# Kernel optimization log

Hardware: AMD Instinct MI355X
Metric: run time of the kernel (lower is better)

Reference implementation:

```python
import jax, jax.numpy as jnp
import numpy as np

B, S, D = 8, 2048, 512

def setup_inputs() -> dict:
    key = jax.random.key(0)
    k1, k2 = jax.random.split(key)
    lstm_out = jax.random.normal(k1, (B, S, D), dtype=jnp.float32)
    # xavier_uniform init for [D, D]
    limit = float(np.sqrt(6.0 / (D + D)))
    attention_weights = jax.random.uniform(k2, (D, D), dtype=jnp.float32, minval=-limit, maxval=limit)
    return {"lstm_out": lstm_out, "attention_weights": attention_weights}

def reference(lstm_out, attention_weights):
    # scores[b,i,j] = tanh( (x W) x^T )
    proj = jnp.einsum('bsd,de->bse', lstm_out, attention_weights)          # [B,S,D]
    scores = jnp.tanh(jnp.einsum('bsd,btd->bst', proj, lstm_out))          # [B,S,S]
    attn = jax.nn.softmax(scores, axis=-1)                                 # [B,S,S]
    return jnp.einsum('bst,btd->bsd', attn, lstm_out)                      # [B,S,D]
```

## Files before the change

kernel.cpp:

```cpp
#include <hip/hip_runtime.h>
#include <hip/hip_bf16.h>

typedef __bf16 bf16;
typedef __attribute__((ext_vector_type(8))) __bf16 bf16x8;
typedef __attribute__((ext_vector_type(4))) __bf16 bf16x4;
typedef __attribute__((ext_vector_type(4))) float floatx4;

__device__ __forceinline__ void gl_lds16(const bf16* g, bf16* l) {
    __builtin_amdgcn_global_load_lds(
        (const __attribute__((address_space(1))) unsigned int*)g,
        (__attribute__((address_space(3))) unsigned int*)l,
        16, 0, 0);
}

__global__ __launch_bounds__(256) void cast_f32_bf16_v4(const float* __restrict__ in,
                                                        bf16* __restrict__ out,
                                                        long long n4) {
    long long i = (long long)blockIdx.x * 256 + threadIdx.x;
    if (i < n4) {
        float4 v = ((const float4*)in)[i];
        bf16x4 o;
        o[0] = (bf16)v.x; o[1] = (bf16)v.y; o[2] = (bf16)v.z; o[3] = (bf16)v.w;
        ((bf16x4*)out)[i] = o;
    }
}

__global__ __launch_bounds__(256) void cast_transpose(const float* __restrict__ in,
                                                      bf16* __restrict__ out,
                                                      int R, int C) {
    __shared__ float tile[32][33];
    const long long bz = blockIdx.z;
    in  += bz * (long long)R * C;
    out += bz * (long long)R * C;
    const int r0 = blockIdx.x * 32, c0 = blockIdx.y * 32;
    const int tx = threadIdx.x & 31, ty = threadIdx.x >> 5;
#pragma unroll
    for (int i = 0; i < 32; i += 8)
        tile[ty + i][tx] = in[(long long)(r0 + ty + i) * C + (c0 + tx)];
    __syncthreads();
#pragma unroll
    for (int i = 0; i < 32; i += 8)
        out[(long long)(c0 + ty + i) * R + (r0 + tx)] = (bf16)tile[tx][ty + i];
}

__device__ __forceinline__ float fast_tanh(float v) {
    float e = __expf(2.0f * v);
    return 1.0f - 2.0f / (e + 1.0f);
}

template <bool TANH, bool OUTBF16>
__global__ __launch_bounds__(256) void gemm128_nt(const bf16* __restrict__ A,
                                                  const bf16* __restrict__ Bm,
                                                  void* __restrict__ Cout,
                                                  int M, int N, int K,
                                                  long long batchA, long long batchB, long long batchC) {
    const long long bz = blockIdx.z;
    A  += bz * batchA;
    Bm += bz * batchB;

    __shared__ bf16 As[128 * 32];
    __shared__ bf16 Bs[128 * 32];

    const int t    = threadIdx.x;
    const int lane = t & 63;
    const int wave = t >> 6;
    const int quad = lane >> 4;
    const int l16  = lane & 15;

    const int m0 = blockIdx.x * 128;
    const int n0 = blockIdx.y * 128;
    const int wm = (wave >> 1) * 64;
    const int wn = (wave & 1) * 64;

    floatx4 acc[4][4] = {};

    const int r0 = t >> 2;
    const int c0 = (t & 3) * 8;

    const bf16* Ag0 = A + (long long)(m0 + r0) * K + c0;
    const bf16* Ag1 = A + (long long)(m0 + 64 + r0) * K + c0;
    const bf16* Bg0 = Bm + (long long)(n0 + r0) * K + c0;
    const bf16* Bg1 = Bm + (long long)(n0 + 64 + r0) * K + c0;

    for (int k0 = 0; k0 < K; k0 += 32) {
        gl_lds16(Ag0 + k0, &As[t * 8]);
        gl_lds16(Ag1 + k0, &As[(t + 256) * 8]);
        gl_lds16(Bg0 + k0, &Bs[t * 8]);
        gl_lds16(Bg1 + k0, &Bs[(t + 256) * 8]);
        __syncthreads();

        bf16x8 af[4], bfr[4];
#pragma unroll
        for (int i = 0; i < 4; ++i)
            af[i] = *(const bf16x8*)(&As[(wm + i * 16 + l16) * 32 + quad * 8]);
#pragma unroll
        for (int j = 0; j < 4; ++j)
            bfr[j] = *(const bf16x8*)(&Bs[(wn + j * 16 + l16) * 32 + quad * 8]);

#pragma unroll
        for (int i = 0; i < 4; ++i)
#pragma unroll
            for (int j = 0; j < 4; ++j)
                acc[i][j] = __builtin_amdgcn_mfma_f32_16x16x32_bf16(af[i], bfr[j], acc[i][j], 0, 0, 0);

        __syncthreads();
    }

#pragma unroll
    for (int i = 0; i < 4; ++i) {
#pragma unroll
        for (int j = 0; j < 4; ++j) {
#pragma unroll
            for (int r = 0; r < 4; ++r) {
                long long row = m0 + wm + i * 16 + quad * 4 + r;
                long long col = n0 + wn + j * 16 + l16;
                float v = acc[i][j][r];
                if (TANH) v = fast_tanh(v);
                if (OUTBF16)
                    ((bf16*)Cout)[bz * batchC + row * (long long)N + col] = (bf16)v;
                else
                    ((float*)Cout)[bz * batchC + row * (long long)N + col] = v;
            }
        }
    }
}

__device__ __forceinline__ float waveRedMax(float v) {
#pragma unroll
    for (int o = 32; o > 0; o >>= 1) v = fmaxf(v, __shfl_xor(v, o));
    return v;
}
__device__ __forceinline__ float waveRedSum(float v) {
#pragma unroll
    for (int o = 32; o > 0; o >>= 1) v += __shfl_xor(v, o);
    return v;
}

__global__ __launch_bounds__(256) void softmax2048(bf16* __restrict__ Sb, long long batchS) {
    bf16* row = Sb + blockIdx.z * batchS + (long long)blockIdx.x * 2048;
    const int t = threadIdx.x;
    const int lane = t & 63, wave = t >> 6;

    bf16x8 pack = ((const bf16x8*)row)[t];
    float v[8];
    float mx = -1e30f;
#pragma unroll
    for (int j = 0; j < 8; ++j) { v[j] = (float)pack[j]; mx = fmaxf(mx, v[j]); }

    __shared__ float smax[4], ssum[4];
    mx = waveRedMax(mx);
    if (lane == 0) smax[wave] = mx;
    __syncthreads();
    mx = fmaxf(fmaxf(smax[0], smax[1]), fmaxf(smax[2], smax[3]));

    float s = 0.f;
#pragma unroll
    for (int j = 0; j < 8; ++j) { v[j] = __expf(v[j] - mx); s += v[j]; }
    s = waveRedSum(s);
    if (lane == 0) ssum[wave] = s;
    __syncthreads();
    s = ssum[0] + ssum[1] + ssum[2] + ssum[3];
    float inv = 1.0f / s;

    bf16x8 o;
#pragma unroll
    for (int j = 0; j < 8; ++j) o[j] = (bf16)(v[j] * inv);
    ((bf16x8*)row)[t] = o;
}

extern "C" void kernel_launch(void* const* d_in, const int* in_sizes, int n_in,
                              void* d_out, int out_size, void* d_ws, size_t ws_size,
                              hipStream_t stream) {
    const int B = 8, S = 2048, D = 512;
    const float* x = (const float*)d_in[0];
    const float* W = (const float*)d_in[1];
    float* out = (float*)d_out;

    const size_t nx = (size_t)B * S * D;
    const size_t nw = (size_t)D * D;

    char* ws = (char*)d_ws;
    auto al = [](size_t v) { return (v + 255) & ~(size_t)255; };
    size_t off = 0;
    bf16* xb = (bf16*)(ws + off); off = al(off + nx * 2);
    bf16* xt = (bf16*)(ws + off); off = al(off + nx * 2);
    bf16* pb = (bf16*)(ws + off); off = al(off + nx * 2);
    bf16* wt = (bf16*)(ws + off); off = al(off + nw * 2);
    bf16* sb = (bf16*)(ws + off);
    const size_t full_need = off + (size_t)B * S * S * 2;
    const bool batched = (ws_size >= full_need);

    cast_f32_bf16_v4<<<(int)((nx / 4 + 255) / 256), 256, 0, stream>>>(x, xb, (long long)(nx / 4));
    { dim3 g(S / 32, D / 32, B); cast_transpose<<<g, 256, 0, stream>>>(x, xt, S, D); }
    { dim3 g(D / 32, D / 32, 1); cast_transpose<<<g, 256, 0, stream>>>(W, wt, D, D); }

    {
        dim3 g(B * S / 128, D / 128, 1);
        gemm128_nt<false, true><<<g, 256, 0, stream>>>(xb, wt, (void*)pb, B * S, D, D, 0, 0, 0);
    }

    const long long sd = (long long)S * D;
    const long long ss = (long long)S * S;

    if (batched) {
        dim3 g2(S / 128, S / 128, B);
        gemm128_nt<true, true><<<g2, 256, 0, stream>>>(pb, xb, (void*)sb, S, S, D, sd, sd, ss);
        dim3 g3(S, 1, B);
        softmax2048<<<g3, 256, 0, stream>>>(sb, ss);
        dim3 g4(S / 128, D / 128, B);
        gemm128_nt<false, false><<<g4, 256, 0, stream>>>(sb, xt, (void*)out, S, D, S, ss, sd, sd);
    } else {
        for (int b = 0; b < B; ++b) {
            dim3 g2(S / 128, S / 128, 1);
            gemm128_nt<true, true><<<g2, 256, 0, stream>>>(pb + (size_t)b * sd, xb + (size_t)b * sd,
                                                          (void*)sb, S, S, D, 0, 0, 0);
            dim3 g3(S, 1, 1);
            softmax2048<<<g3, 256, 0, stream>>>(sb, 0);
            dim3 g4(S / 128, D / 128, 1);
            gemm128_nt<false, false><<<g4, 256, 0, stream>>>(sb, xt + (size_t)b * sd,
                                                             (void*)(out + (size_t)b * sd), S, D, S, 0, 0, 0);
        }
    }
}
```

Measured before the change: 248.0 us.

## Fuse softmax into score GEMM epilogue with atomic row sums and deferred normalization

Drops the separate softmax kernel. The score GEMM now writes exp(tanh(s)) and atomically accumulates per-row sums, and the output GEMM divides by the row sum in its epilogue. This is safe without max subtraction because tanh bounds the scores to [-1,1]. Both epilogues are also staged through LDS so global stores are coalesced and vectorized. The cost is extra atomics, a memset, and a larger LDS allocation that may reduce occupancy.

New measurement: 248.8 us. About the same (+0.3%).

```diff
diff --git a/kernel.cpp b/kernel.cpp
--- a/kernel.cpp
+++ b/kernel.cpp
@@ -48,18 +48,21 @@
     return 1.0f - 2.0f / (e + 1.0f);
 }
 
-template <bool TANH, bool OUTBF16>
+template <int MODE>
 __global__ __launch_bounds__(256) void gemm128_nt(const bf16* __restrict__ A,
                                                   const bf16* __restrict__ Bm,
                                                   void* __restrict__ Cout,
+                                                  float* __restrict__ rowsum,
                                                   int M, int N, int K,
-                                                  long long batchA, long long batchB, long long batchC) {
+                                                  long long batchA, long long batchB,
+                                                  long long batchC, long long batchR) {
     const long long bz = blockIdx.z;
     A  += bz * batchA;
     Bm += bz * batchB;
 
-    __shared__ bf16 As[128 * 32];
-    __shared__ bf16 Bs[128 * 32];
+    __shared__ __align__(16) char lds_raw[34816];
+    bf16* As = (bf16*)lds_raw;
+    bf16* Bs = As + 128 * 32;
 
     const int t    = threadIdx.x;
     const int lane = t & 63;
@@ -106,66 +109,77 @@
         __syncthreads();
     }
 
-#pragma unroll
-    for (int i = 0; i < 4; ++i) {
-#pragma unroll
-        for (int j = 0; j < 4; ++j) {
-#pragma unroll
-            for (int r = 0; r < 4; ++r) {
-                long long row = m0 + wm + i * 16 + quad * 4 + r;
-                long long col = n0 + wn + j * 16 + l16;
-                float v = acc[i][j][r];
-                if (TANH) v = fast_tanh(v);
-                if (OUTBF16)
-                    ((bf16*)Cout)[bz * batchC + row * (long long)N + col] = (bf16)v;
-                else
-                    ((float*)Cout)[bz * batchC + row * (long long)N + col] = v;
+    if (MODE == 0 || MODE == 1) {
+        bf16* Cb = (bf16*)lds_raw;
+        float ps[4][4];
+#pragma unroll
+        for (int i = 0; i < 4; ++i)
+#pragma unroll
+            for (int r = 0; r < 4; ++r) ps[i][r] = 0.f;
+
+#pragma unroll
+        for (int i = 0; i < 4; ++i)
+#pragma unroll
+            for (int j = 0; j < 4; ++j)
+#pragma unroll
+                for (int r = 0; r < 4; ++r) {
+                    float v = acc[i][j][r];
+                    if (MODE == 1) { v = __expf(fast_tanh(v)); ps[i][r] += v; }
+                    Cb[(wm + i * 16 + quad * 4 + r) * 136 + (wn + j * 16 + l16)] = (bf16)v;
+                }
+
+        if (MODE == 1) {
+#pragma unroll
+            for (int i = 0; i < 4; ++i)
+#pragma unroll
+                for (int r = 0; r < 4; ++r) {
+                    float s = ps[i][r];
+#pragma unroll
+                    for (int msk = 1; msk < 16; msk <<= 1) s += __shfl_xor(s, msk);
+                    if (l16 == 0)
+                        atomicAdd(&rowsum[bz * batchR + m0 + wm + i * 16 + quad * 4 + r], s);
+                }
+        }
+        __syncthreads();
+        bf16* Cg = (bf16*)Cout + bz * batchC;
+#pragma unroll
+        for (int c = 0; c < 8; ++c) {
+            int ch  = t + c * 256;
+            int row = ch >> 4, k16 = ch & 15;
+            bf16x8 pk = *(const bf16x8*)&Cb[row * 136 + k16 * 8];
+            *(bf16x8*)(Cg + (long long)(m0 + row) * N + n0 + k16 * 8) = pk;
+        }
+    } else {
+        float* Cf = (float*)lds_raw;
+        float* rs = (float*)lds_raw + 64 * 132;
+        if (t < 128) rs[t] = rowsum[bz * batchR + m0 + t];
+        __syncthreads();
+        float* Og = (float*)Cout + bz * batchC;
+#pragma unroll
+        for (int half = 0; half < 2; ++half) {
+            if (wm == half * 64) {
+#pragma unroll
+                for (int i = 0; i < 4; ++i)
+#pragma unroll
+                    for (int r = 0; r < 4; ++r) {
+                        int rl = i * 16 + quad * 4 + r;
+                        float inv = 1.0f / rs[half * 64 + rl];
+#pragma unroll
+                        for (int j = 0; j < 4; ++j)
+                            Cf[rl * 132 + (wn + j * 16 + l16)] = acc[i][j][r] * inv;
+                    }
             }
-        }
-    }
-}
-
-__device__ __forceinline__ float waveRedMax(float v) {
-#pragma unroll
-    for (int o = 32; o > 0; o >>= 1) v = fmaxf(v, __shfl_xor(v, o));
-    return v;
-}
-__device__ __forceinline__ float waveRedSum(float v) {
-#pragma unroll
-    for (int o = 32; o > 0; o >>= 1) v += __shfl_xor(v, o);
-    return v;
-}
-
-__global__ __launch_bounds__(256) void softmax2048(bf16* __restrict__ Sb, long long batchS) {
-    bf16* row = Sb + blockIdx.z * batchS + (long long)blockIdx.x * 2048;
-    const int t = threadIdx.x;
-    const int lane = t & 63, wave = t >> 6;
-
-    bf16x8 pack = ((const bf16x8*)row)[t];
-    float v[8];
-    float mx = -1e30f;
-#pragma unroll
-    for (int j = 0; j < 8; ++j) { v[j] = (float)pack[j]; mx = fmaxf(mx, v[j]); }
-
-    __shared__ float smax[4], ssum[4];
-    mx = waveRedMax(mx);
-    if (lane == 0) smax[wave] = mx;
-    __syncthreads();
-    mx = fmaxf(fmaxf(smax[0], smax[1]), fmaxf(smax[2], smax[3]));
-
-    float s = 0.f;
-#pragma unroll
-    for (int j = 0; j < 8; ++j) { v[j] = __expf(v[j] - mx); s += v[j]; }
-    s = waveRedSum(s);
-    if (lane == 0) ssum[wave] = s;
-    __syncthreads();
-    s = ssum[0] + ssum[1] + ssum[2] + ssum[3];
-    float inv = 1.0f / s;
-
-    bf16x8 o;
-#pragma unroll
-    for (int j = 0; j < 8; ++j) o[j] = (bf16)(v[j] * inv);
-    ((bf16x8*)row)[t] = o;
+            __syncthreads();
+#pragma unroll
+            for (int c = 0; c < 8; ++c) {
+                int ch  = t + c * 256;
+                int row = ch >> 5, c4 = ch & 31;
+                floatx4 pk = *(const floatx4*)&Cf[row * 132 + c4 * 4];
+                *(floatx4*)(Og + (long long)(m0 + half * 64 + row) * N + n0 + c4 * 4) = pk;
+            }
+            __syncthreads();
+        }
+    }
 }
 
 extern "C" void kernel_launch(void* const* d_in, const int* in_sizes, int n_in,
@@ -186,17 +200,20 @@
     bf16* xt = (bf16*)(ws + off); off = al(off + nx * 2);
     bf16* pb = (bf16*)(ws + off); off = al(off + nx * 2);
     bf16* wt = (bf16*)(ws + off); off = al(off + nw * 2);
+    float* rsum = (float*)(ws + off); off = al(off + (size_t)B * S * 4);
     bf16* sb = (bf16*)(ws + off);
     const size_t full_need = off + (size_t)B * S * S * 2;
     const bool batched = (ws_size >= full_need);
 
+    hipMemsetAsync(rsum, 0, (size_t)B * S * 4, stream);
+
     cast_f32_bf16_v4<<<(int)((nx / 4 + 255) / 256), 256, 0, stream>>>(x, xb, (long long)(nx / 4));
     { dim3 g(S / 32, D / 32, B); cast_transpose<<<g, 256, 0, stream>>>(x, xt, S, D); }
     { dim3 g(D / 32, D / 32, 1); cast_transpose<<<g, 256, 0, stream>>>(W, wt, D, D); }
 
     {
         dim3 g(B * S / 128, D / 128, 1);
-        gemm128_nt<false, true><<<g, 256, 0, stream>>>(xb, wt, (void*)pb, B * S, D, D, 0, 0, 0);
+        gemm128_nt<0><<<g, 256, 0, stream>>>(xb, wt, (void*)pb, nullptr, B * S, D, D, 0, 0, 0, 0);
     }
 
     const long long sd = (long long)S * D;
@@ -204,21 +221,18 @@
 
     if (batched) {
         dim3 g2(S / 128, S / 128, B);
-        gemm128_nt<true, true><<<g2, 256, 0, stream>>>(pb, xb, (void*)sb, S, S, D, sd, sd, ss);
-        dim3 g3(S, 1, B);
-        softmax2048<<<g3, 256, 0, stream>>>(sb, ss);
+        gemm128_nt<1><<<g2, 256, 0, stream>>>(pb, xb, (void*)sb, rsum, S, S, D, sd, sd, ss, S);
         dim3 g4(S / 128, D / 128, B);
-        gemm128_nt<false, false><<<g4, 256, 0, stream>>>(sb, xt, (void*)out, S, D, S, ss, sd, sd);
+        gemm128_nt<2><<<g4, 256, 0, stream>>>(sb, xt, (void*)out, rsum, S, D, S, ss, sd, sd, S);
     } else {
         for (int b = 0; b < B; ++b) {
             dim3 g2(S / 128, S / 128, 1);
-            gemm128_nt<true, true><<<g2, 256, 0, stream>>>(pb + (size_t)b * sd, xb + (size_t)b * sd,
-                                                          (void*)sb, S, S, D, 0, 0, 0);
-            dim3 g3(S, 1, 1);
-            softmax2048<<<g3, 256, 0, stream>>>(sb, 0);
+            gemm128_nt<1><<<g2, 256, 0, stream>>>(pb + (size_t)b * sd, xb + (size_t)b * sd,
+                                                  (void*)sb, rsum + (size_t)b * S, S, S, D, 0, 0, 0, 0);
             dim3 g4(S / 128, D / 128, 1);
-            gemm128_nt<false, false><<<g4, 256, 0, stream>>>(sb, xt + (size_t)b * sd,
-                                                             (void*)(out + (size_t)b * sd), S, D, S, 0, 0, 0);
-        }
-    }
-}
+            gemm128_nt<2><<<g4, 256, 0, stream>>>(sb, xt + (size_t)b * sd,
+                                                  (void*)(out + (size_t)b * sd), rsum + (size_t)b * S,
+                                                  S, D, S, 0, 0, 0, 0);
+        }
+    }
+}
```
